# Optimization experiments

Measured on AMD Instinct MI355X. Metric: run time of the kernel, lower is better.

The kernel has to match this reference:

```python
import jax, jax.numpy as jnp
import numpy as np

N = 100000   # nodes
E = 1200000  # directed edges
F_IN, HID, EMB = 5, 64, 16

def setup_inputs() -> dict:
    key = jax.random.key(0)
    ks = jax.random.split(key, 12)
    # node features: [lambda, mu, is_comp, is_AND, is_OR]
    lam = jax.random.uniform(ks[0], (N, 1), jnp.float32) * 0.01
    mu = jax.random.uniform(ks[1], (N, 1), jnp.float32) * 0.1
    node_type = jax.random.randint(ks[2], (N,), 0, 3)
    onehot = jax.nn.one_hot(node_type, 3, dtype=jnp.float32)
    x = jnp.concatenate([lam, mu, onehot], axis=1)  # [N,5]
    edge_index = jax.random.randint(ks[3], (2, E), 0, N, dtype=jnp.int32)

    def lin(k, fi, fo):
        s = 1.0 / np.sqrt(fi)
        return jax.random.uniform(k, (fi, fo), jnp.float32, -s, s)

    return {
        "x": x, "edge_index": edge_index,
        "T": jnp.float32(100.0), "T_max": jnp.float32(500.0),
        "W1": lin(ks[4], F_IN, HID), "b1": jnp.zeros((HID,), jnp.float32),
        "W2": lin(ks[5], HID, HID), "b2": jnp.zeros((HID,), jnp.float32),
        "W3": lin(ks[6], HID, EMB), "b3": jnp.zeros((EMB,), jnp.float32),
        "P1": lin(ks[7], EMB + 8, 64), "pb1": jnp.zeros((64,), jnp.float32),
        "P2": lin(ks[8], 64, 32), "pb2": jnp.zeros((32,), jnp.float32),
        "P3": lin(ks[9], 32, 4), "pb3": jnp.zeros((4,), jnp.float32),
    }

def gcn_conv(h_in, src, dst, W, b):
    """PyG GCNConv: add self-loops, symmetric D^-1/2 (A+I) D^-1/2 norm."""
    h = h_in @ W  # [N,F]
    # degree with self-loops: 1 + in-degree (count on target nodes)
    deg = jax.ops.segment_sum(jnp.ones((E,), jnp.float32), dst, num_segments=N) + 1.0
    dinv = jax.lax.rsqrt(deg)  # [N]
    norm = dinv[src] * dinv[dst]  # [E]
    agg = jax.ops.segment_sum(h[src] * norm[:, None], dst, num_segments=N)
    agg = agg + h * (dinv * dinv)[:, None]  # self-loop term norm = 1/deg
    return agg + b

def reference(x, edge_index, T, T_max, W1, b1, W2, b2, W3, b3,
              P1, pb1, P2, pb2, P3, pb3):
    src, dst = edge_index[0], edge_index[1]
    h = jax.nn.relu(gcn_conv(x, src, dst, W1, b1))
    h = jax.nn.relu(gcn_conv(h, src, dst, W2, b2))
    h = gcn_conv(h, src, dst, W3, b3)
    embedding = jnp.mean(h, axis=0, keepdims=True)  # global_mean_pool, batch=0 -> [1,EMB]

    T_norm = T / T_max
    comp = x[:, 2]
    n_comp = jnp.sum(comp)
    n_AND = jnp.sum(x[:, 3])
    n_OR = jnp.sum(x[:, 4])
    safe = jnp.maximum(n_comp, 1.0)
    has = n_comp > 0
    avg_lambda = jnp.where(has, jnp.sum(x[:, 0] * comp) / safe, 0.0)
    avg_mu = jnp.where(has, jnp.sum(x[:, 1] * comp) / safe, 0.0)
    t_inv = 1.0 / (1.0 + T_norm)
    gf = jnp.stack([n_comp, n_AND, n_OR, n_AND + n_OR,
                    avg_lambda, avg_mu, T_norm * 50.0, t_inv * 50.0])[None, :]  # [1,8]

    emb = jnp.concatenate([embedding, gf], axis=1)  # [1,24]
    hmlp = jax.nn.relu(emb @ P1 + pb1)
    hmlp = jax.nn.relu(hmlp @ P2 + pb2)
    raw = hmlp @ P3 + pb3  # [1,4]

    val = jax.nn.softplus(raw + 2.0)
    alpha_min = 1.0 + val[:, 0]
    alpha_max = alpha_min + val[:, 1] + 0.5
    beta_min = 1.0 + val[:, 2]
    beta_max = beta_min + val[:, 3] + 0.5
    out = jnp.stack([alpha_min, alpha_max, beta_min, beta_max], axis=1)  # [1,4]
    return out, emb
```

## Files before the change

kernel.cpp:

```cpp
#include <hip/hip_runtime.h>

#define NN 100000
#define NE 1200000
#define NB_SCAN ((NN + 255) / 256)
#define NPASS 8
#define WNODES ((NN + NPASS - 1) / NPASS)
#define EB 128
#define GF_BLOCKS 64
#define WS_BLOCKS 256

__global__ void k_hist(const int* __restrict__ ei, int* __restrict__ cnt) {
    int i = blockIdx.x * 256 + threadIdx.x;
    if (i < NE) atomicAdd(&cnt[ei[NE + i]], 1);
}

__global__ void k_colw(const int* __restrict__ ei, const float* __restrict__ dinv,
                       float* __restrict__ colw) {
    int e = blockIdx.x * 256 + threadIdx.x;
    if (e < NE) atomicAdd(&colw[ei[e]], dinv[ei[NE + e]]);
}

__global__ void k_scan_block(const int* __restrict__ cnt, int* __restrict__ incl,
                             int* __restrict__ bsum, float* __restrict__ dinv) {
    __shared__ int s[256];
    int t = threadIdx.x;
    int i = blockIdx.x * 256 + t;
    int v = (i < NN) ? cnt[i] : 0;
    if (i < NN) dinv[i] = rsqrtf((float)v + 1.0f);
    s[t] = v;
    __syncthreads();
    for (int off = 1; off < 256; off <<= 1) {
        int add = (t >= off) ? s[t - off] : 0;
        __syncthreads();
        s[t] += add;
        __syncthreads();
    }
    if (i < NN) incl[i] = s[t];
    if (t == 255) bsum[blockIdx.x] = s[255];
}

__global__ void k_scan_bsum(int* __restrict__ bsum) {
    __shared__ int s[512];
    int t = threadIdx.x;
    s[t] = (t < NB_SCAN) ? bsum[t] : 0;
    __syncthreads();
    for (int off = 1; off < 512; off <<= 1) {
        int add = (t >= off) ? s[t - off] : 0;
        __syncthreads();
        s[t] += add;
        __syncthreads();
    }
    if (t < NB_SCAN) bsum[t] = s[t];
}

__global__ void k_scan_add(const int* __restrict__ cnt, const int* __restrict__ incl,
                           const int* __restrict__ bsum, int* __restrict__ rowptr) {
    int i = blockIdx.x * 256 + threadIdx.x;
    if (i >= NN) return;
    int base = (blockIdx.x > 0) ? bsum[blockIdx.x - 1] : 0;
    rowptr[i] = base + incl[i] - cnt[i];
    if (i == 0) rowptr[NN] = NE;
}

__global__ void k_scatter_win(const int* __restrict__ ei, const int* __restrict__ rowptr,
                              int* __restrict__ cursor, int* __restrict__ srcs) {
    int pass = blockIdx.x & (NPASS - 1);
    int blk  = blockIdx.x / NPASS;
    int lo = pass * WNODES;
    int hi = lo + WNODES;
    for (int e = blk * 256 + threadIdx.x; e < NE; e += EB * 256) {
        int dst = ei[NE + e];
        if (dst >= lo && dst < hi) {
            int pos = rowptr[dst] + atomicAdd(&cursor[dst], 1);
            srcs[pos] = ei[e];
        }
    }
}

__global__ void k_aggx(const int* __restrict__ rowptr, const int* __restrict__ srcs,
                       const float* __restrict__ dinv, const float* __restrict__ x,
                       float* __restrict__ aggx) {
    int t = threadIdx.x;
    int n = blockIdx.x * 4 + (t >> 6);
    if (n >= NN) return;
    int lane = t & 63, c = lane & 7, slot = lane >> 3;
    int e0 = rowptr[n], e1 = rowptr[n + 1];
    float es = 0.f;
    if (c < 5) {
        for (int j = e0 + slot; j < e1; j += 8) {
            int s = srcs[j];
            es += x[(size_t)s * 5 + c] * dinv[s];
        }
    }
    es += __shfl_xor(es, 8, 64);
    es += __shfl_xor(es, 16, 64);
    es += __shfl_xor(es, 32, 64);
    float dvn = dinv[n];
    if (slot == 0 && c < 5)
        aggx[(size_t)n * 5 + c] = es * dvn + x[(size_t)n * 5 + c] * dvn * dvn;
}

__global__ void k_lin_first(const float* __restrict__ aggx, const float* __restrict__ W,
                            const float* __restrict__ b, float* __restrict__ h) {
    __shared__ float Ws[5 * 64];
    __shared__ float bs[64];
    int t = threadIdx.x;
    for (int i = t; i < 320; i += 256) Ws[i] = W[i];
    if (t < 64) bs[t] = b[t];
    __syncthreads();
    int r = t >> 6, c = t & 63;
    int row = blockIdx.x * 4 + r;
    if (row >= NN) return;
    float acc = bs[c];
#pragma unroll
    for (int k = 0; k < 5; k++) acc += aggx[(size_t)row * 5 + k] * Ws[k * 64 + c];
    h[(size_t)row * 64 + c] = fmaxf(acc, 0.f);
}

__global__ void k_lin64(const float* __restrict__ in, const float* __restrict__ W,
                        float* __restrict__ h) {
    __shared__ float Ws[64 * 64];
    __shared__ float rows[256];
    int t = threadIdx.x;
    for (int i = t; i < 4096; i += 256) Ws[i] = W[i];
    int base = blockIdx.x * 4;
    int gidx = base * 64 + t;
    rows[t] = (gidx < NN * 64) ? in[gidx] : 0.f;
    __syncthreads();
    int r = t >> 6, c = t & 63, row = base + r;
    if (row >= NN) return;
    float acc = 0.f;
#pragma unroll
    for (int k = 0; k < 64; k++) acc += rows[r * 64 + k] * Ws[k * 64 + c];
    h[(size_t)row * 64 + c] = acc;
}

template <bool RELU>
__global__ void k_agg64(const int* __restrict__ rowptr, const int* __restrict__ srcs,
                        const float* __restrict__ dinv, const float* __restrict__ h,
                        const float* __restrict__ b, float* __restrict__ out) {
    int t = threadIdx.x;
    int n = blockIdx.x * 4 + (t >> 6);
    if (n >= NN) return;
    int c = t & 63;
    int e0 = rowptr[n], e1 = rowptr[n + 1];
    float dvn = dinv[n];
    float acc0 = 0.f, acc1 = 0.f, acc2 = 0.f, acc3 = 0.f;
    int j = e0;
    for (; j + 3 < e1; j += 4) {
        int s0 = srcs[j], s1 = srcs[j + 1], s2 = srcs[j + 2], s3 = srcs[j + 3];
        float w0 = dinv[s0], w1 = dinv[s1], w2 = dinv[s2], w3 = dinv[s3];
        acc0 += h[(size_t)s0 * 64 + c] * w0;
        acc1 += h[(size_t)s1 * 64 + c] * w1;
        acc2 += h[(size_t)s2 * 64 + c] * w2;
        acc3 += h[(size_t)s3 * 64 + c] * w3;
    }
    for (; j < e1; j++) {
        int s0 = srcs[j];
        acc0 += h[(size_t)s0 * 64 + c] * dinv[s0];
    }
    float v = ((acc0 + acc1) + (acc2 + acc3)) * dvn
            + h[(size_t)n * 64 + c] * dvn * dvn + b[c];
    if (RELU) v = fmaxf(v, 0.f);
    out[(size_t)n * 64 + c] = v;
}

__global__ void k_wsum(const float* __restrict__ h2, const float* __restrict__ colw,
                       const float* __restrict__ dinv, float* __restrict__ part) {
    int t = threadIdx.x;
    int c = t & 63;
    float acc = 0.f;
    for (int r = blockIdx.x * 4 + (t >> 6); r < NN; r += WS_BLOCKS * 4) {
        float dv = dinv[r];
        acc += dv * (colw[r] + dv) * h2[(size_t)r * 64 + c];
    }
    __shared__ float s[256];
    s[t] = acc;
    __syncthreads();
    if (t < 128) s[t] += s[t + 128];
    __syncthreads();
    if (t < 64) part[blockIdx.x * 64 + t] = s[t] + s[t + 64];
}

__global__ void k_gf_part(const float* __restrict__ x, float* __restrict__ gfpart) {
    int t = threadIdx.x;
    float sc = 0, sa = 0, so = 0, sl = 0, sm = 0;
    for (int i = blockIdx.x * 256 + t; i < NN; i += gridDim.x * 256) {
        float lam = x[i * 5 + 0], mu = x[i * 5 + 1];
        float c = x[i * 5 + 2], a = x[i * 5 + 3], o = x[i * 5 + 4];
        sc += c; sa += a; so += o; sl += lam * c; sm += mu * c;
    }
    __shared__ float s[256];
    float vals[5] = {sc, sa, so, sl, sm};
#pragma unroll
    for (int k = 0; k < 5; k++) {
        s[t] = vals[k];
        __syncthreads();
        for (int off = 128; off > 0; off >>= 1) {
            if (t < off) s[t] += s[t + off];
            __syncthreads();
        }
        if (t == 0) gfpart[blockIdx.x * 5 + k] = s[0];
        __syncthreads();
    }
}

__device__ __forceinline__ float softplus_f(float x) {
    return (x > 20.f) ? x : log1pf(expf(x));
}

__global__ void k_mlp(const float* __restrict__ part64, const float* __restrict__ gfpart,
                      const float* __restrict__ W3, const float* __restrict__ b3,
                      const float* __restrict__ T, const float* __restrict__ Tmax,
                      const float* __restrict__ P1, const float* __restrict__ pb1,
                      const float* __restrict__ P2, const float* __restrict__ pb2,
                      const float* __restrict__ P3, const float* __restrict__ pb3,
                      float* __restrict__ out) {
    __shared__ float sf[256][4];
    __shared__ float Ws3[64 * 16];
    __shared__ float gfs[GF_BLOCKS][5];
    __shared__ float m[64];
    __shared__ float emb[24];
    __shared__ float hm1[64];
    __shared__ float hm2[32];
    __shared__ float val[4];
    int t = threadIdx.x;

    for (int i = t; i < 1024; i += 256) Ws3[i] = W3[i];
    if (t < GF_BLOCKS) {
#pragma unroll
        for (int k = 0; k < 5; k++) gfs[t][k] = gfpart[t * 5 + k];
    }

    {
        const float4* p4 = (const float4*)part64;
        int f4c = t & 15, g = t >> 4;
        float4 a = make_float4(0.f, 0.f, 0.f, 0.f);
#pragma unroll
        for (int k = 0; k < WS_BLOCKS / 16; k++) {
            float4 v = p4[(g + k * 16) * 16 + f4c];
            a.x += v.x; a.y += v.y; a.z += v.z; a.w += v.w;
        }
        sf[t][0] = a.x; sf[t][1] = a.y; sf[t][2] = a.z; sf[t][3] = a.w;
        __syncthreads();
        for (int off = 128; off >= 16; off >>= 1) {
            if (t < off) {
#pragma unroll
                for (int j = 0; j < 4; j++) sf[t][j] += sf[t + off][j];
            }
            __syncthreads();
        }
        if (t < 16) {
#pragma unroll
            for (int j = 0; j < 4; j++) m[t * 4 + j] = sf[t][j];
        }
        __syncthreads();
    }
    if (t < 16) {
        float acc = 0.f;
#pragma unroll
        for (int c = 0; c < 64; c++) acc += m[c] * Ws3[c * 16 + t];
        emb[t] = acc / (float)NN + b3[t];
    }
    if (t >= 32 && t < 37) {
        int k = t - 32;
        float acc = 0.f;
        for (int r = 0; r < GF_BLOCKS; r++) acc += gfs[r][k];
        sf[0][0 * 0];
        gfs[0][k] = acc;
    }
    __syncthreads();
    if (t == 0) {
        float sc = gfs[0][0], sa = gfs[0][1], so = gfs[0][2], sl = gfs[0][3], sm = gfs[0][4];
        float Tn = T[0] / Tmax[0];
        emb[16] = sc;
        emb[17] = sa;
        emb[18] = so;
        emb[19] = sa + so;
        float safe = fmaxf(sc, 1.0f);
        bool has = sc > 0.f;
        emb[20] = has ? sl / safe : 0.f;
        emb[21] = has ? sm / safe : 0.f;
        emb[22] = Tn * 50.f;
        emb[23] = (1.f / (1.f + Tn)) * 50.f;
    }
    __syncthreads();
    if (t < 64) {
        float acc = pb1[t];
#pragma unroll
        for (int k = 0; k < 24; k++) acc += emb[k] * P1[k * 64 + t];
        hm1[t] = fmaxf(acc, 0.f);
    }
    __syncthreads();
    if (t < 32) {
        float acc = pb2[t];
#pragma unroll
        for (int k = 0; k < 64; k++) acc += hm1[k] * P2[k * 32 + t];
        hm2[t] = fmaxf(acc, 0.f);
    }
    __syncthreads();
    if (t < 4) {
        float acc = pb3[t];
#pragma unroll
        for (int k = 0; k < 32; k++) acc += hm2[k] * P3[k * 4 + t];
        val[t] = softplus_f(acc + 2.0f);
    }
    __syncthreads();
    if (t == 0) {
        float amin = 1.f + val[0];
        float amax = amin + val[1] + 0.5f;
        float bmin = 1.f + val[2];
        float bmax = bmin + val[3] + 0.5f;
        out[0] = amin; out[1] = amax; out[2] = bmin; out[3] = bmax;
    }
    if (t >= 4 && t < 28) out[t] = emb[t - 4];
}

extern "C" void kernel_launch(void* const* d_in, const int* in_sizes, int n_in,
                              void* d_out, int out_size, void* d_ws, size_t ws_size,
                              hipStream_t stream) {
    const float* x    = (const float*)d_in[0];
    const int*   ei   = (const int*)d_in[1];
    const float* T    = (const float*)d_in[2];
    const float* Tmax = (const float*)d_in[3];
    const float* W1   = (const float*)d_in[4];
    const float* b1   = (const float*)d_in[5];
    const float* W2   = (const float*)d_in[6];
    const float* b2   = (const float*)d_in[7];
    const float* W3   = (const float*)d_in[8];
    const float* b3   = (const float*)d_in[9];
    const float* P1   = (const float*)d_in[10];
    const float* pb1  = (const float*)d_in[11];
    const float* P2   = (const float*)d_in[12];
    const float* pb2  = (const float*)d_in[13];
    const float* P3   = (const float*)d_in[14];
    const float* pb3  = (const float*)d_in[15];
    float* out = (float*)d_out;

    char* w = (char*)d_ws;
    float* bufH   = (float*)w;                 w += (size_t)NN * 64 * 4;
    float* bufA   = (float*)w;                 w += (size_t)NN * 64 * 4;
    int*   cnt    = (int*)w;                   w += (size_t)NN * 4;
    int*   cursor = (int*)w;                   w += (size_t)NN * 4;
    float* colw   = (float*)w;                 w += (size_t)NN * 4;
    float* dinv   = (float*)w;                 w += (size_t)NN * 4;
    int*   incl   = (int*)w;                   w += (size_t)NN * 4;
    int*   rowptr = (int*)w;                   w += (size_t)(NN + 1) * 4;
    int*   srcs   = (int*)w;                   w += (size_t)NE * 4;
    int*   bsum   = (int*)w;                   w += 512 * 4;
    float* aggx   = (float*)w;                 w += (size_t)NN * 5 * 4;
    w = (char*)(((size_t)w + 15) & ~(size_t)15);
    float* part64 = (float*)w;                 w += (size_t)WS_BLOCKS * 64 * 4;
    float* gfpart = (float*)w;                 w += (size_t)GF_BLOCKS * 5 * 4;

    hipMemsetAsync(cnt, 0, 3 * (size_t)NN * sizeof(int), stream);

    k_hist<<<(NE + 255) / 256, 256, 0, stream>>>(ei, cnt);
    k_scan_block<<<NB_SCAN, 256, 0, stream>>>(cnt, incl, bsum, dinv);
    k_scan_bsum<<<1, 512, 0, stream>>>(bsum);
    k_scan_add<<<NB_SCAN, 256, 0, stream>>>(cnt, incl, bsum, rowptr);
    k_scatter_win<<<NPASS * EB, 256, 0, stream>>>(ei, rowptr, cursor, srcs);
    k_colw<<<(NE + 255) / 256, 256, 0, stream>>>(ei, dinv, colw);

    k_aggx<<<(NN + 3) / 4, 256, 0, stream>>>(rowptr, srcs, dinv, x, aggx);
    k_lin_first<<<(NN + 3) / 4, 256, 0, stream>>>(aggx, W1, b1, bufA);

    k_lin64<<<(NN + 3) / 4, 256, 0, stream>>>(bufA, W2, bufH);
    k_agg64<true><<<(NN + 3) / 4, 256, 0, stream>>>(rowptr, srcs, dinv, bufH, b2, bufA);

    k_wsum<<<WS_BLOCKS, 256, 0, stream>>>(bufA, colw, dinv, part64);

    k_gf_part<<<GF_BLOCKS, 256, 0, stream>>>(x, gfpart);
    k_mlp<<<1, 256, 0, stream>>>(part64, gfpart, W3, b3, T, Tmax,
                                 P1, pb1, P2, pb2, P3, pb3, out);
}
```

Before: 470.6 us.

## Replace global atomic histogram/scatter/colw with LDS-windowed per-block partials

```diff
diff --git a/kernel.cpp b/kernel.cpp
--- a/kernel.cpp
+++ b/kernel.cpp
@@ -4,20 +4,40 @@
 #define NE 1200000
 #define NB_SCAN ((NN + 255) / 256)
 #define NPASS 8
-#define WNODES ((NN + NPASS - 1) / NPASS)
-#define EB 128
+#define WNODES 12500
+#define NBW 32
 #define GF_BLOCKS 64
 #define WS_BLOCKS 256
 
-__global__ void k_hist(const int* __restrict__ ei, int* __restrict__ cnt) {
-    int i = blockIdx.x * 256 + threadIdx.x;
-    if (i < NE) atomicAdd(&cnt[ei[NE + i]], 1);
-}
-
-__global__ void k_colw(const int* __restrict__ ei, const float* __restrict__ dinv,
-                       float* __restrict__ colw) {
-    int e = blockIdx.x * 256 + threadIdx.x;
-    if (e < NE) atomicAdd(&colw[ei[e]], dinv[ei[NE + e]]);
+__global__ void k_hist_part(const int* __restrict__ ei, int* __restrict__ hpart) {
+    __shared__ int lh[WNODES];
+    int w = blockIdx.x / NBW, b = blockIdx.x % NBW;
+    int t = threadIdx.x;
+    for (int i = t; i < WNODES; i += 256) lh[i] = 0;
+    __syncthreads();
+    int lo = w * WNODES;
+    for (int e = b * 256 + t; e < NE; e += NBW * 256) {
+        unsigned d = (unsigned)(ei[NE + e] - lo);
+        if (d < WNODES) atomicAdd(&lh[d], 1);
+    }
+    __syncthreads();
+    int* dp = hpart + (size_t)blockIdx.x * WNODES;
+    for (int i = t; i < WNODES; i += 256) dp[i] = lh[i];
+}
+
+__global__ void k_hist_merge(int* __restrict__ hpart, int* __restrict__ cnt) {
+    int n = blockIdx.x * 256 + threadIdx.x;
+    if (n >= NN) return;
+    int w = n / WNODES, i = n % WNODES;
+    size_t base = (size_t)w * NBW * WNODES + i;
+    int run = 0;
+    for (int b = 0; b < NBW; b++) {
+        size_t idx = base + (size_t)b * WNODES;
+        int v = hpart[idx];
+        hpart[idx] = run;
+        run += v;
+    }
+    cnt[n] = run;
 }
 
 __global__ void k_scan_block(const int* __restrict__ cnt, int* __restrict__ incl,
@@ -62,19 +82,50 @@
     if (i == 0) rowptr[NN] = NE;
 }
 
-__global__ void k_scatter_win(const int* __restrict__ ei, const int* __restrict__ rowptr,
-                              int* __restrict__ cursor, int* __restrict__ srcs) {
-    int pass = blockIdx.x & (NPASS - 1);
-    int blk  = blockIdx.x / NPASS;
-    int lo = pass * WNODES;
-    int hi = lo + WNODES;
-    for (int e = blk * 256 + threadIdx.x; e < NE; e += EB * 256) {
+__global__ void k_scatter_nb(const int* __restrict__ ei, const int* __restrict__ rowptr,
+                             const int* __restrict__ hpart, int* __restrict__ srcs) {
+    __shared__ int lcur[WNODES];
+    int w = blockIdx.x / NBW, b = blockIdx.x % NBW;
+    int t = threadIdx.x;
+    const int* pp = hpart + (size_t)blockIdx.x * WNODES;
+    for (int i = t; i < WNODES; i += 256) lcur[i] = pp[i];
+    __syncthreads();
+    int lo = w * WNODES;
+    for (int e = b * 256 + t; e < NE; e += NBW * 256) {
         int dst = ei[NE + e];
-        if (dst >= lo && dst < hi) {
-            int pos = rowptr[dst] + atomicAdd(&cursor[dst], 1);
-            srcs[pos] = ei[e];
-        }
-    }
+        unsigned d = (unsigned)(dst - lo);
+        if (d < WNODES) {
+            int pos = atomicAdd(&lcur[d], 1);
+            srcs[rowptr[dst] + pos] = ei[e];
+        }
+    }
+}
+
+__global__ void k_colw_part(const int* __restrict__ ei, const float* __restrict__ dinv,
+                            float* __restrict__ cpart) {
+    __shared__ float lc[WNODES];
+    int w = blockIdx.x / NBW, b = blockIdx.x % NBW;
+    int t = threadIdx.x;
+    for (int i = t; i < WNODES; i += 256) lc[i] = 0.f;
+    __syncthreads();
+    int lo = w * WNODES;
+    for (int e = b * 256 + t; e < NE; e += NBW * 256) {
+        unsigned d = (unsigned)(ei[e] - lo);
+        if (d < WNODES) atomicAdd(&lc[d], dinv[ei[NE + e]]);
+    }
+    __syncthreads();
+    float* dp = cpart + (size_t)blockIdx.x * WNODES;
+    for (int i = t; i < WNODES; i += 256) dp[i] = lc[i];
+}
+
+__global__ void k_colw_merge(const float* __restrict__ cpart, float* __restrict__ colw) {
+    int n = blockIdx.x * 256 + threadIdx.x;
+    if (n >= NN) return;
+    int w = n / WNODES, i = n % WNODES;
+    size_t base = (size_t)w * NBW * WNODES + i;
+    float run = 0.f;
+    for (int b = 0; b < NBW; b++) run += cpart[base + (size_t)b * WNODES];
+    colw[n] = run;
 }
 
 __global__ void k_aggx(const int* __restrict__ rowptr, const int* __restrict__ srcs,
@@ -266,7 +317,6 @@
         int k = t - 32;
         float acc = 0.f;
         for (int r = 0; r < GF_BLOCKS; r++) acc += gfs[r][k];
-        sf[0][0 * 0];
         gfs[0][k] = acc;
     }
     __syncthreads();
@@ -341,7 +391,6 @@
     float* bufH   = (float*)w;                 w += (size_t)NN * 64 * 4;
     float* bufA   = (float*)w;                 w += (size_t)NN * 64 * 4;
     int*   cnt    = (int*)w;                   w += (size_t)NN * 4;
-    int*   cursor = (int*)w;                   w += (size_t)NN * 4;
     float* colw   = (float*)w;                 w += (size_t)NN * 4;
     float* dinv   = (float*)w;                 w += (size_t)NN * 4;
     int*   incl   = (int*)w;                   w += (size_t)NN * 4;
@@ -353,14 +402,17 @@
     float* part64 = (float*)w;                 w += (size_t)WS_BLOCKS * 64 * 4;
     float* gfpart = (float*)w;                 w += (size_t)GF_BLOCKS * 5 * 4;
 
-    hipMemsetAsync(cnt, 0, 3 * (size_t)NN * sizeof(int), stream);
-
-    k_hist<<<(NE + 255) / 256, 256, 0, stream>>>(ei, cnt);
+    int*   hpart = (int*)bufH;
+    float* cpart = (float*)(bufH + (size_t)NPASS * NBW * WNODES);
+
+    k_hist_part<<<NPASS * NBW, 256, 0, stream>>>(ei, hpart);
+    k_hist_merge<<<NB_SCAN, 256, 0, stream>>>(hpart, cnt);
     k_scan_block<<<NB_SCAN, 256, 0, stream>>>(cnt, incl, bsum, dinv);
     k_scan_bsum<<<1, 512, 0, stream>>>(bsum);
     k_scan_add<<<NB_SCAN, 256, 0, stream>>>(cnt, incl, bsum, rowptr);
-    k_scatter_win<<<NPASS * EB, 256, 0, stream>>>(ei, rowptr, cursor, srcs);
-    k_colw<<<(NE + 255) / 256, 256, 0, stream>>>(ei, dinv, colw);
+    k_scatter_nb<<<NPASS * NBW, 256, 0, stream>>>(ei, rowptr, hpart, srcs);
+    k_colw_part<<<NPASS * NBW, 256, 0, stream>>>(ei, dinv, cpart);
+    k_colw_merge<<<NB_SCAN, 256, 0, stream>>>(cpart, colw);
 
     k_aggx<<<(NN + 3) / 4, 256, 0, stream>>>(rowptr, srcs, dinv, x, aggx);
     k_lin_first<<<(NN + 3) / 4, 256, 0, stream>>>(aggx, W1, b1, bufA);
```

Measured after the change: 535.1 us. 13.7% more time.
